# Performance work log

Measured on AMD Instinct MI355X. Metric: run time of the kernel, lower is better.

Reference implementation:

```python
import jax, jax.numpy as jnp
import numpy as np

B, F_IN, F_OUT = 256, 1024, 1024


def setup_inputs() -> dict:
    key = jax.random.key(0)
    ks = jax.random.split(key, 7)
    return {
        "x": jax.random.normal(ks[0], (B, F_IN), dtype=jnp.float32),
        "weight_mu": jax.random.normal(ks[1], (F_OUT, F_IN), dtype=jnp.float32) * 0.05,
        "weight_rho": jax.random.normal(ks[2], (F_OUT, F_IN), dtype=jnp.float32) - 5.0,
        "bias_mu": jax.random.normal(ks[3], (F_OUT,), dtype=jnp.float32) * 0.05,
        "bias_rho": jax.random.normal(ks[4], (F_OUT,), dtype=jnp.float32) - 5.0,
        "eps_w": jax.random.normal(ks[5], (B, F_OUT, F_IN), dtype=jnp.float32),
        "eps_b": jax.random.normal(ks[6], (B, F_OUT), dtype=jnp.float32),
    }


def reference(x, weight_mu, weight_rho, bias_mu, bias_rho, eps_w, eps_b):
    # Reparameterized per-sample weights: w_b = mu + softplus(rho) * eps_b
    # weight: (B, F_OUT, F_IN) -- the large intermediate the fused kernel avoids
    weight = weight_mu[None, :, :] + jax.nn.softplus(weight_rho)[None, :, :] * eps_w
    # batched vec-matmul: (B,1,F_IN) @ (B,F_IN,F_OUT) -> (B,F_OUT)
    y = jnp.einsum('bi,boi->bo', x, weight)
    bias = bias_mu[None, :] + jax.nn.softplus(bias_rho)[None, :] * eps_b  # (B, F_OUT)
    return y + bias
```

## Files before the change

### kernel.cpp

```cpp
#include <hip/hip_runtime.h>
#include <math.h>

#define BATCH 256
#define FIN   1024
#define FOUT  1024

typedef float f4 __attribute__((ext_vector_type(4)));

__device__ __forceinline__ float softplus_f(float x) {
    return fmaxf(x, 0.0f) + log1pf(expf(-fabsf(x)));
}

__global__ void __launch_bounds__(256) sp_precompute(const float* __restrict__ rho,
                                                     float* __restrict__ sw) {
    int i = (blockIdx.x * 256 + threadIdx.x) * 4;
    f4 r = *(const f4*)(rho + i);
    f4 s;
    s.x = softplus_f(r.x);
    s.y = softplus_f(r.y);
    s.z = softplus_f(r.z);
    s.w = softplus_f(r.w);
    *(f4*)(sw + i) = s;
}

template <bool PRE>
__global__ void __launch_bounds__(256) bayes_linear_main(
    const float* __restrict__ x,
    const float* __restrict__ mu,
    const float* __restrict__ swrho,
    const float* __restrict__ bmu,
    const float* __restrict__ brho,
    const float* __restrict__ eps_w,
    const float* __restrict__ eps_b,
    float* __restrict__ out)
{
    const int wave = (blockIdx.x << 2) + (threadIdx.x >> 6);
    const int lane = threadIdx.x & 63;
    const int b = wave >> 10;
    const int o = wave & (FOUT - 1);

    const float* xr  = x     + (size_t)b * FIN;
    const float* mur = mu    + (size_t)o * FIN;
    const float* swr = swrho + (size_t)o * FIN;
    const float* er  = eps_w + (size_t)wave * FIN;

    float acc = 0.0f;
#pragma unroll
    for (int c = 0; c < 4; ++c) {
        const int idx = c * 256 + lane * 4;
        f4 xe = *(const f4*)(xr  + idx);
        f4 me = *(const f4*)(mur + idx);
        f4 se = *(const f4*)(swr + idx);
        f4 ee = __builtin_nontemporal_load((const f4*)(er + idx));

        if (!PRE) {
            se.x = softplus_f(se.x);
            se.y = softplus_f(se.y);
            se.z = softplus_f(se.z);
            se.w = softplus_f(se.w);
        }

        acc = fmaf(xe.x, fmaf(se.x, ee.x, me.x), acc);
        acc = fmaf(xe.y, fmaf(se.y, ee.y, me.y), acc);
        acc = fmaf(xe.z, fmaf(se.z, ee.z, me.z), acc);
        acc = fmaf(xe.w, fmaf(se.w, ee.w, me.w), acc);
    }

#pragma unroll
    for (int off = 32; off > 0; off >>= 1)
        acc += __shfl_xor(acc, off, 64);

    if (lane == 0) {
        float bias = bmu[o] + softplus_f(brho[o]) * eps_b[wave];
        out[wave] = acc + bias;
    }
}

extern "C" void kernel_launch(void* const* d_in, const int* in_sizes, int n_in,
                              void* d_out, int out_size, void* d_ws, size_t ws_size,
                              hipStream_t stream) {
    const float* x     = (const float*)d_in[0];
    const float* wmu   = (const float*)d_in[1];
    const float* wrho  = (const float*)d_in[2];
    const float* bmu   = (const float*)d_in[3];
    const float* brho  = (const float*)d_in[4];
    const float* eps_w = (const float*)d_in[5];
    const float* eps_b = (const float*)d_in[6];
    float* out = (float*)d_out;

    const size_t sw_bytes = (size_t)FOUT * FIN * sizeof(float);
    const int n_pairs = BATCH * FOUT;
    const int main_blocks = n_pairs / 4;

    if (ws_size >= sw_bytes) {
        float* sw = (float*)d_ws;
        sp_precompute<<<(FOUT * FIN) / (256 * 4), 256, 0, stream>>>(wrho, sw);
        bayes_linear_main<true><<<main_blocks, 256, 0, stream>>>(
            x, wmu, sw, bmu, brho, eps_w, eps_b, out);
    } else {
        bayes_linear_main<false><<<main_blocks, 256, 0, stream>>>(
            x, wmu, wrho, bmu, brho, eps_w, eps_b, out);
    }
}
```

Baseline: 1.429 ms.

## Fuse softplus into main kernel and process four batch rows per wave

Drops the separate softplus precompute pass and computes softplus of rho inline. Each wave now handles one output feature across four batch rows, so the mu and softplus(rho) values it loads and computes are reused four times. The aim is to remove an extra kernel launch and the workspace round-trip, and to cut mu/rho traffic against the eps_w stream, which dominates. In exchange there is more transcendental work per wave and more registers in use, and each wave reads four widely strided eps_w rows.

```diff
diff --git a/kernel.cpp b/kernel.cpp
--- a/kernel.cpp
+++ b/kernel.cpp
@@ -11,68 +11,85 @@
     return fmaxf(x, 0.0f) + log1pf(expf(-fabsf(x)));
 }
 
-__global__ void __launch_bounds__(256) sp_precompute(const float* __restrict__ rho,
-                                                     float* __restrict__ sw) {
-    int i = (blockIdx.x * 256 + threadIdx.x) * 4;
-    f4 r = *(const f4*)(rho + i);
+__device__ __forceinline__ f4 softplus_v(f4 r) {
     f4 s;
     s.x = softplus_f(r.x);
     s.y = softplus_f(r.y);
     s.z = softplus_f(r.z);
     s.w = softplus_f(r.w);
-    *(f4*)(sw + i) = s;
+    return s;
 }
 
-template <bool PRE>
-__global__ void __launch_bounds__(256) bayes_linear_main(
+__device__ __forceinline__ float dot_acc(f4 xv, f4 se, f4 ev, f4 me, float acc) {
+    acc = fmaf(xv.x, fmaf(se.x, ev.x, me.x), acc);
+    acc = fmaf(xv.y, fmaf(se.y, ev.y, me.y), acc);
+    acc = fmaf(xv.z, fmaf(se.z, ev.z, me.z), acc);
+    acc = fmaf(xv.w, fmaf(se.w, ev.w, me.w), acc);
+    return acc;
+}
+
+__global__ void __launch_bounds__(256) bayes_linear_fused(
     const float* __restrict__ x,
     const float* __restrict__ mu,
-    const float* __restrict__ swrho,
+    const float* __restrict__ rho,
     const float* __restrict__ bmu,
     const float* __restrict__ brho,
     const float* __restrict__ eps_w,
     const float* __restrict__ eps_b,
     float* __restrict__ out)
 {
-    const int wave = (blockIdx.x << 2) + (threadIdx.x >> 6);
+    const int warp = threadIdx.x >> 6;
     const int lane = threadIdx.x & 63;
-    const int b = wave >> 10;
-    const int o = wave & (FOUT - 1);
+    const int bg   = blockIdx.x >> 8;
+    const int o    = ((blockIdx.x & 255) << 2) | warp;
+    const int b0   = bg << 2;
 
-    const float* xr  = x     + (size_t)b * FIN;
-    const float* mur = mu    + (size_t)o * FIN;
-    const float* swr = swrho + (size_t)o * FIN;
-    const float* er  = eps_w + (size_t)wave * FIN;
+    const float* mur = mu  + (size_t)o * FIN;
+    const float* rhr = rho + (size_t)o * FIN;
+    const float* xr  = x   + (size_t)b0 * FIN;
+    const float* er  = eps_w + ((size_t)b0 * FOUT + o) * FIN;
+    const size_t BSTRIDE = (size_t)FOUT * FIN;
 
-    float acc = 0.0f;
+    float a0 = 0.0f, a1 = 0.0f, a2 = 0.0f, a3 = 0.0f;
+
 #pragma unroll
     for (int c = 0; c < 4; ++c) {
         const int idx = c * 256 + lane * 4;
-        f4 xe = *(const f4*)(xr  + idx);
+
         f4 me = *(const f4*)(mur + idx);
-        f4 se = *(const f4*)(swr + idx);
-        f4 ee = __builtin_nontemporal_load((const f4*)(er + idx));
+        f4 se = softplus_v(*(const f4*)(rhr + idx));
 
-        if (!PRE) {
-            se.x = softplus_f(se.x);
-            se.y = softplus_f(se.y);
-            se.z = softplus_f(se.z);
-            se.w = softplus_f(se.w);
-        }
+        f4 x0 = *(const f4*)(xr + idx);
+        f4 x1 = *(const f4*)(xr + FIN + idx);
+        f4 x2 = *(const f4*)(xr + 2 * FIN + idx);
+        f4 x3 = *(const f4*)(xr + 3 * FIN + idx);
 
-        acc = fmaf(xe.x, fmaf(se.x, ee.x, me.x), acc);
-        acc = fmaf(xe.y, fmaf(se.y, ee.y, me.y), acc);
-        acc = fmaf(xe.z, fmaf(se.z, ee.z, me.z), acc);
-        acc = fmaf(xe.w, fmaf(se.w, ee.w, me.w), acc);
+        f4 e0 = __builtin_nontemporal_load((const f4*)(er + idx));
+        f4 e1 = __builtin_nontemporal_load((const f4*)(er + BSTRIDE + idx));
+        f4 e2 = __builtin_nontemporal_load((const f4*)(er + 2 * BSTRIDE + idx));
+        f4 e3 = __builtin_nontemporal_load((const f4*)(er + 3 * BSTRIDE + idx));
+
+        a0 = dot_acc(x0, se, e0, me, a0);
+        a1 = dot_acc(x1, se, e1, me, a1);
+        a2 = dot_acc(x2, se, e2, me, a2);
+        a3 = dot_acc(x3, se, e3, me, a3);
     }
 
 #pragma unroll
-    for (int off = 32; off > 0; off >>= 1)
-        acc += __shfl_xor(acc, off, 64);
+    for (int off = 32; off > 0; off >>= 1) {
+        a0 += __shfl_xor(a0, off, 64);
+        a1 += __shfl_xor(a1, off, 64);
+        a2 += __shfl_xor(a2, off, 64);
+        a3 += __shfl_xor(a3, off, 64);
+    }
 
     if (lane == 0) {
-        float bias = bmu[o] + softplus_f(brho[o]) * eps_b[wave];
-        out[wave] = acc + bias;
+        const float bm = bmu[o];
+        const float sb = softplus_f(brho[o]);
+        out[(size_t)(b0 + 0) * FOUT + o] = a0 + bm + sb * eps_b[(size_t)(b0 + 0) * FOUT + o];
+        out[(size_t)(b0 + 1) * FOUT + o] = a1 + bm + sb * eps_b[(size_t)(b0 + 1) * FOUT + o];
+        out[(size_t)(b0 + 2) * FOUT + o] = a2 + bm + sb * eps_b[(size_t)(b0 + 2) * FOUT + o];
+        out[(size_t)(b0 + 3) * FOUT + o] = a3 + bm + sb * eps_b[(size_t)(b0 + 3) * FOUT + o];
     }
 }
 
@@ -88,17 +105,9 @@
     const float* eps_b = (const float*)d_in[6];
     float* out = (float*)d_out;
 
-    const size_t sw_bytes = (size_t)FOUT * FIN * sizeof(float);
-    const int n_pairs = BATCH * FOUT;
-    const int main_blocks = n_pairs / 4;
+    (void)d_ws; (void)ws_size;
 
-    if (ws_size >= sw_bytes) {
-        float* sw = (float*)d_ws;
-        sp_precompute<<<(FOUT * FIN) / (256 * 4), 256, 0, stream>>>(wrho, sw);
-        bayes_linear_main<true><<<main_blocks, 256, 0, stream>>>(
-            x, wmu, sw, bmu, brho, eps_w, eps_b, out);
-    } else {
-        bayes_linear_main<false><<<main_blocks, 256, 0, stream>>>(
-            x, wmu, wrho, bmu, brho, eps_w, eps_b, out);
-    }
+    const int blocks = (BATCH / 4) * (FOUT / 4);
+    bayes_linear_fused<<<blocks, 256, 0, stream>>>(
+        x, wmu, wrho, bmu, brho, eps_w, eps_b, out);
 }
```

New measurement: 1.338 ms. -6.3%, faster.
